# Kernel tuning notes

Hardware: AMD Instinct MI355X
Metric: run time of the kernel (lower is better)

The kernel has to match this reference:

```python
import jax, jax.numpy as jnp
import numpy as np

SPARQ = 32
NEG = -32000.0


def sparq_masked_bmm(a, b, xs, xs_mask, value):
    # a: [N,A,B], b: [N,C,B], xs/xs_mask: [N,A,Z]
    N, A, B = a.shape
    C = b.shape[1]
    xs = jnp.clip(xs, 0, C - 1)
    _, a_idx = jax.lax.top_k(jnp.abs(a), SPARQ)              # SparQ: keep top-32 |q| dims
    a_mask = jnp.zeros_like(a).at[
        jnp.arange(N)[:, None, None], jnp.arange(A)[None, :, None], a_idx].set(1.0)
    ts = jnp.einsum('nab,ncb->nac', a * a_mask, b)           # [N,A,C]
    ys = jnp.take_along_axis(ts, xs, axis=-1)                # [N,A,Z]
    return jnp.where(xs_mask > 0.5, ys, value)


def forward_mask(w0, k_budget, q, k):
    # q: [NH, A, HID], k: [NH, T_SRC, HID]; returns additive mask [NH, A, T_SRC]
    NH, A, HID = q.shape
    T_SRC = k.shape[1]
    start = T_SRC - A + 1
    tsrcs_f = jnp.arange(start, start + A).astype(jnp.float32)   # [A]
    ws = jnp.full((A,), float(w0), jnp.float32)
    Zc = 2 * k_budget + 8                                        # static cap on unique pixel count
    z = jnp.arange(Zc)
    pixels = jnp.broadcast_to(jnp.where(z < k_budget, z, 0)[None, None, :], (NH, A, Zc)).astype(jnp.int32)
    pmask = jnp.broadcast_to((z < w0).astype(jnp.float32)[None, None, :], (NH, A, Zc))
    need = (ws < tsrcs_f)[None, :, None]                         # computed ONCE, as in torch
    w = w0
    while True:  # static python loop: w doubles until T_SRC
        txs = jnp.round(pixels * (tsrcs_f / ws)[None, :, None]).astype(jnp.int32)
        scores = sparq_masked_bmm(q, k, txs, pmask, NEG)
        tks = jnp.clip(jnp.round(ws / tsrcs_f * k_budget), 1.0,
                       jnp.minimum(ws - 1.0, float(Zc - 1))).astype(jnp.int32)[None, :, None]
        _, idx = jax.lax.top_k(scores, Zc)
        new_pixels = jnp.take_along_axis(pixels, idx, axis=-1)
        new_mask = (z[None, None, :] < tks).astype(jnp.float32)
        pixels = jnp.where(need, new_pixels, pixels)
        pmask = jnp.where(need, new_mask, pmask)
        # tree doubling: each pixel splits into up to 2 children at the new scale
        ws_new = jnp.minimum(tsrcs_f, ws * 2.0)
        scale = (ws_new / ws)[None, :, None]
        ps_start = jnp.round(pixels * scale).astype(jnp.int32)
        ps_end = jnp.round((pixels + 1) * scale).astype(jnp.int32)
        counts = ps_end - ps_start
        reps = jnp.arange(2, dtype=jnp.float32)[None, None, None, :] * pmask[..., None]
        reps = jnp.minimum(reps, jnp.maximum(counts - 1, 0)[..., None].astype(jnp.float32)).astype(jnp.int32)
        ps = (ps_start[..., None] + reps).reshape(NH * A, Zc * 2)
        # emulate sort + unique_consecutive + compacting scatter (duplicates -> -1 tail)
        ps = jnp.sort(ps, axis=-1)
        is_new = jnp.concatenate([jnp.ones((NH * A, 1), bool), ps[:, 1:] != ps[:, :-1]], axis=1)
        rank = jnp.cumsum(is_new, axis=-1) - 1
        res = jnp.full_like(ps, -1).at[jnp.arange(NH * A)[:, None], rank].set(ps)
        res = res.reshape(NH, A, 2 * Zc)[:, :, :Zc]              # static truncation (valid count <= 2k+1)
        pmask = (res >= 0).astype(jnp.float32)
        pixels = jnp.where(res >= 0, res, 0)
        ws = ws_new
        if w == T_SRC:
            break
        w = min(T_SRC, w * 2)
    pixels = (pixels.astype(jnp.float32) * pmask).astype(jnp.int32)
    ret = jnp.full((NH, A, T_SRC), NEG, jnp.float32)
    ret = ret.at[jnp.arange(NH)[:, None, None], jnp.arange(A)[None, :, None], pixels].set(0.0)
    return ret


def tree_attention(q, k, v, mask, k_budget, w0):
    N, H, T_SRC, HID = k.shape
    T_DST = q.shape[2]
    t_dense = max(0, k_budget - T_SRC + T_DST)
    outs = []
    if t_dense > 0:
        s = jnp.einsum('nhqd,nhkd->nhqk', q[:, :, :t_dense], k) + mask[:, :, :t_dense]
        outs.append(jnp.einsum('nhqk,nhkd->nhqd', jax.nn.softmax(s, axis=-1), v))
    if T_DST - t_dense > 0:
        qs = q[:, :, t_dense:]
        ms = forward_mask(w0, k_budget,
                          qs.reshape(N * H, -1, HID),
                          k.reshape(N * H, T_SRC, HID)).reshape(N, H, -1, T_SRC)
        s = jnp.einsum('nhqd,nhkd->nhqk', qs, k) + mask[:, :, t_dense:] + ms
        outs.append(jnp.einsum('nhqk,nhkd->nhqd', jax.nn.softmax(s, axis=-1), v))
    return jnp.concatenate(outs, axis=2)


def setup_inputs():
    key = jax.random.key(0)
    kq, kk, kv = jax.random.split(key, 3)
    N, H, T, HID = 1, 8, 2048, 64
    q = jax.random.normal(kq, (N, H, T, HID), jnp.float32)
    k = jax.random.normal(kk, (N, H, T, HID), jnp.float32)
    v = jax.random.normal(kv, (N, H, T, HID), jnp.float32)
    causal = jnp.tril(jnp.ones((T, T), bool))
    mask = jnp.where(causal, 0.0, NEG)[None, None].astype(jnp.float32)
    return {"q": q, "k": k, "v": v, "mask": mask}


def reference(q, k, v, mask):
    return tree_attention(q, k, v, mask, 512, 64)
```

## Files before the change

kernel.cpp:

```cpp
#include <hip/hip_runtime.h>
#include <math.h>

constexpr int HID    = 64;
constexpr int TT     = 2048;
constexpr int NHEAD  = 8;
constexpr int TDENSE = 512;
constexpr int ZC     = 1032;
constexpr int BITW   = 1024;

__device__ __forceinline__ float waveSum(float v) {
#pragma unroll
    for (int o = 32; o > 0; o >>= 1) v += __shfl_xor(v, o, 64);
    return v;
}
__device__ __forceinline__ int waveSumI(int v) {
#pragma unroll
    for (int o = 32; o > 0; o >>= 1) v += __shfl_xor(v, o, 64);
    return v;
}
__device__ __forceinline__ float waveMax(float v) {
#pragma unroll
    for (int o = 32; o > 0; o >>= 1) v = fmaxf(v, __shfl_xor(v, o, 64));
    return v;
}
__device__ __forceinline__ unsigned orderKey(float f) {
    unsigned u = __float_as_uint(f);
    return (u & 0x80000000u) ? ~u : (u | 0x80000000u);
}
__device__ __forceinline__ float dot4(float4 a, float4 b) {
    return fmaf(a.x, b.x, fmaf(a.y, b.y, fmaf(a.z, b.z, a.w * b.w)));
}
__device__ __forceinline__ float dotRow64(const float4* __restrict__ kr,
                                          const float4* __restrict__ qs) {
    float s0 = 0.f, s1 = 0.f, s2 = 0.f, s3 = 0.f;
#pragma unroll 2
    for (int i = 0; i < 4; i++) {
        float4 ka = kr[4*i+0], kb = kr[4*i+1], kc = kr[4*i+2], kd = kr[4*i+3];
        float4 qa = qs[4*i+0], qb = qs[4*i+1], qc = qs[4*i+2], qd = qs[4*i+3];
        s0 += dot4(ka, qa); s1 += dot4(kb, qb);
        s2 += dot4(kc, qc); s3 += dot4(kd, qd);
    }
    return (s0 + s1) + (s2 + s3);
}

struct __align__(16) SMem {
    float qf[HID];
    float aq[HID];
    float qm[HID];
    float partial[256];
    unsigned short pixA[ZC];
    unsigned short pixB[ZC];
    unsigned skey[ZC];
    unsigned bitmap[BITW];
    unsigned hist[256];
    float red[8];
    int scal[8];
    unsigned wsum[4];
};

__global__ __launch_bounds__(256)
void tree_attn_kernel(const float* __restrict__ q, const float* __restrict__ k,
                      const float* __restrict__ v, float* __restrict__ out) {
    __shared__ SMem sm;
    const int t    = blockIdx.x;
    const int h    = blockIdx.y;
    const int tid  = threadIdx.x;
    const int lane = tid & 63;
    const int wave = tid >> 6;
    const int sub  = lane & 15;
    const int grp  = lane >> 4;

    const float* qrow = q + (size_t)(h * TT + t) * HID;
    const float* kh   = k + (size_t)h * TT * HID;
    const float* vh   = v + (size_t)h * TT * HID;
    float*       orow = out + (size_t)(h * TT + t) * HID;

    if (tid < HID) sm.qf[tid] = qrow[tid];
    __syncthreads();

    if (t < TDENSE) {
        const int nk = t + 1;
        float* f = (float*)sm.skey;
        for (int z = tid; z < nk; z += 256)
            f[z] = dotRow64((const float4*)(kh + (size_t)z * HID), (const float4*)sm.qf);
        __syncthreads();
        float m = -3.0e38f;
        for (int z = tid; z < nk; z += 256) m = fmaxf(m, f[z]);
        m = waveMax(m);
        if (lane == 0) sm.red[wave] = m;
        __syncthreads();
        m = fmaxf(fmaxf(sm.red[0], sm.red[1]), fmaxf(sm.red[2], sm.red[3]));
        __syncthreads();
        float ls = 0.f;
        for (int z = tid; z < nk; z += 256) { float e = expf(f[z] - m); f[z] = e; ls += e; }
        ls = waveSum(ls);
        if (lane == 0) sm.red[4 + wave] = ls;
        __syncthreads();
        ls = sm.red[4] + sm.red[5] + sm.red[6] + sm.red[7];
        float4 acc = {0.f, 0.f, 0.f, 0.f};
        for (int z = (wave << 2) + grp; z < nk; z += 16) {
            float w = f[z];
            const float4 vv = *reinterpret_cast<const float4*>(vh + (size_t)z * HID + (sub << 2));
            acc.x = fmaf(w, vv.x, acc.x); acc.y = fmaf(w, vv.y, acc.y);
            acc.z = fmaf(w, vv.z, acc.z); acc.w = fmaf(w, vv.w, acc.w);
        }
#pragma unroll
        for (int o = 16; o <= 32; o <<= 1) {
            acc.x += __shfl_xor(acc.x, o, 64); acc.y += __shfl_xor(acc.y, o, 64);
            acc.z += __shfl_xor(acc.z, o, 64); acc.w += __shfl_xor(acc.w, o, 64);
        }
        if (grp == 0) reinterpret_cast<float4*>(sm.partial)[wave * 16 + sub] = acc;
        __syncthreads();
        if (tid < HID) {
            float o = sm.partial[tid] + sm.partial[64 + tid] + sm.partial[128 + tid] + sm.partial[192 + tid];
            orow[tid] = o / ls;
        }
        return;
    }

    const int a     = t - TDENSE;
    const int tsrci = TDENSE + 1 + a;
    const float tsrc = (float)tsrci;

    if (tid < HID) sm.aq[tid] = fabsf(sm.qf[tid]);
    __syncthreads();
    if (tid < HID) {
        float me = sm.aq[tid]; int c = 0;
#pragma unroll
        for (int i = 0; i < HID; i++) {
            float o = sm.aq[i];
            c += (o > me) || (o == me && i < tid);
        }
        sm.qm[tid] = (c < 32) ? sm.qf[tid] : 0.0f;
    }
    for (int z = tid; z < ZC; z += 256) sm.pixA[z] = (z < 512) ? (unsigned short)z : (unsigned short)0;
    __syncthreads();

    unsigned short* cur = sm.pixA;
    unsigned short* nxt = sm.pixB;
    int U = 64;
    float ws = 64.0f;
    int pmaxb = 511;

    for (int it = 0; it < 6; it++) {
        if (ws == tsrc) break;
        const float wsn   = fminf(tsrc, ws * 2.0f);
        const float ratio = tsrc / ws;

        for (int z = tid; z < U; z += 256) {
            int p  = cur[z];
            int tx = (int)rintf((float)p * ratio);
            tx = min(max(tx, 0), TT - 1);
            float s = dotRow64((const float4*)(kh + (size_t)tx * HID), (const float4*)sm.qm);
            sm.skey[z] = orderKey(s);
        }
        float tkf = rintf((ws / tsrc) * 512.0f);
        tkf = fminf(fmaxf(tkf, 1.0f), fminf(ws - 1.0f, 1031.0f));
        const int tks = (int)tkf;
        __syncthreads();

        unsigned thr = 0u;
        if (tks < U) {
            if (tid == 0) { sm.scal[0] = tks; sm.scal[1] = 0; }
            __syncthreads();
            for (int bs = 24; bs >= 0; bs -= 8) {
                sm.hist[tid] = 0;
                __syncthreads();
                const unsigned pref = (unsigned)sm.scal[1];
                for (int z = tid; z < U; z += 256) {
                    unsigned key = sm.skey[z];
                    bool ok = (bs == 24) || ((key >> (bs + 8)) == (pref >> (bs + 8)));
                    if (ok) atomicAdd(&sm.hist[(key >> bs) & 255u], 1u);
                }
                __syncthreads();
                if (wave == 0) {
                    int c0 = (int)sm.hist[4*lane+0], c1 = (int)sm.hist[4*lane+1];
                    int c2 = (int)sm.hist[4*lane+2], c3 = (int)sm.hist[4*lane+3];
                    int tsum = c0 + c1 + c2 + c3;
                    int x = tsum;
#pragma unroll
                    for (int o = 1; o < 64; o <<= 1) {
                        int y = __shfl_up(x, o, 64);
                        if (lane >= o) x += y;
                    }
                    const int T   = __shfl(x, 63, 64);
                    const int wnt = sm.scal[0];
                    const int R   = T - wnt;
                    int p3 = x, p2 = p3 - c3, p1 = p2 - c2, p0 = p1 - c1, pm1 = p0 - c0;
                    int b = -1, nw = 0, cc = 0;
                    if      (p0 > R && pm1 <= R) { b = 4*lane+0; nw = p0 - R; cc = c0; }
                    else if (p1 > R && p0  <= R) { b = 4*lane+1; nw = p1 - R; cc = c1; }
                    else if (p2 > R && p1  <= R) { b = 4*lane+2; nw = p2 - R; cc = c2; }
                    else if (p3 > R && p2  <= R) { b = 4*lane+3; nw = p3 - R; cc = c3; }
                    if (b >= 0) {
                        sm.scal[0] = nw;
                        sm.scal[1] = (int)(pref | ((unsigned)b << bs));
                        sm.scal[2] = cc;
                    }
                }
                __syncthreads();
                if (sm.scal[2] == sm.scal[0]) break;
            }
            thr = (unsigned)sm.scal[1];
        }

        const float scale = wsn / ws;
        const int pmax_new = min(32767, (int)rintf((float)(pmaxb + 1) * scale));
        const int nwords = (pmax_new >> 5) + 1;
        for (int w0 = tid; w0 < nwords; w0 += 256) sm.bitmap[w0] = 0;
        __syncthreads();
        for (int z = tid; z < ZC; z += 256) {
            int p = cur[z];
            float pf = (float)p;
            int ps0 = (int)rintf(pf * scale);
            ps0 = min(ps0, 32767);
            atomicOr(&sm.bitmap[ps0 >> 5], 1u << (ps0 & 31));
            if (z < U && sm.skey[z] >= thr) {
                int ps1 = (int)rintf((pf + 1.0f) * scale);
                if (ps1 - ps0 >= 2) {
                    int ch = min(ps0 + 1, 32767);
                    atomicOr(&sm.bitmap[ch >> 5], 1u << (ch & 31));
                }
            }
        }
        __syncthreads();

        const int base = tid * 4;
        unsigned b0 = (base + 0 < nwords) ? sm.bitmap[base + 0] : 0u;
        unsigned b1 = (base + 1 < nwords) ? sm.bitmap[base + 1] : 0u;
        unsigned b2 = (base + 2 < nwords) ? sm.bitmap[base + 2] : 0u;
        unsigned b3 = (base + 3 < nwords) ? sm.bitmap[base + 3] : 0u;
        int myc = __popc(b0) + __popc(b1) + __popc(b2) + __popc(b3);
        int x = myc;
#pragma unroll
        for (int o = 1; o < 64; o <<= 1) {
            int y = __shfl_up(x, o, 64);
            if (lane >= o) x += y;
        }
        if (lane == 63) sm.wsum[wave] = (unsigned)x;
        __syncthreads();
        int wOff = 0;
        for (int wv = 0; wv < wave; wv++) wOff += (int)sm.wsum[wv];
        const int total = (int)(sm.wsum[0] + sm.wsum[1] + sm.wsum[2] + sm.wsum[3]);
        const int newU = min(total, ZC);
        int pos = wOff + x - myc;
#pragma unroll
        for (int w0 = 0; w0 < 4; w0++) {
            unsigned bits = (w0 == 0) ? b0 : (w0 == 1) ? b1 : (w0 == 2) ? b2 : b3;
            int vbase = (base + w0) << 5;
            while (bits) {
                int b = __ffs(bits) - 1;
                bits &= bits - 1;
                if (pos < ZC) nxt[pos] = (unsigned short)(vbase + b);
                pos++;
            }
        }
        for (int z = newU + tid; z < ZC; z += 256) nxt[z] = 0;
        __syncthreads();

        unsigned short* tmp = cur; cur = nxt; nxt = tmp;
        U = newU;
        ws = wsn;
        pmaxb = pmax_new;
    }

    int ca = 0;
    for (int z = tid; z < U; z += 256) ca += (cur[z] < tsrci) ? 1 : 0;
    ca = waveSumI(ca);
    if (lane == 0) sm.scal[wave] = ca;
    __syncthreads();
    const int Uatt = sm.scal[0] + sm.scal[1] + sm.scal[2] + sm.scal[3];
    __syncthreads();

    float* f = (float*)sm.skey;
    for (int z = tid; z < Uatt; z += 256)
        f[z] = dotRow64((const float4*)(kh + (size_t)cur[z] * HID), (const float4*)sm.qf);
    __syncthreads();
    float m = -3.0e38f;
    for (int z = tid; z < Uatt; z += 256) m = fmaxf(m, f[z]);
    m = waveMax(m);
    if (lane == 0) sm.red[wave] = m;
    __syncthreads();
    m = fmaxf(fmaxf(sm.red[0], sm.red[1]), fmaxf(sm.red[2], sm.red[3]));
    __syncthreads();
    float ls = 0.f;
    for (int z = tid; z < Uatt; z += 256) { float e = expf(f[z] - m); f[z] = e; ls += e; }
    ls = waveSum(ls);
    if (lane == 0) sm.red[4 + wave] = ls;
    __syncthreads();
    ls = sm.red[4] + sm.red[5] + sm.red[6] + sm.red[7];
    float4 acc = {0.f, 0.f, 0.f, 0.f};
    for (int z = (wave << 2) + grp; z < Uatt; z += 16) {
        float w = f[z];
        const float4 vv = *reinterpret_cast<const float4*>(vh + (size_t)cur[z] * HID + (sub << 2));
        acc.x = fmaf(w, vv.x, acc.x); acc.y = fmaf(w, vv.y, acc.y);
        acc.z = fmaf(w, vv.z, acc.z); acc.w = fmaf(w, vv.w, acc.w);
    }
#pragma unroll
    for (int o = 16; o <= 32; o <<= 1) {
        acc.x += __shfl_xor(acc.x, o, 64); acc.y += __shfl_xor(acc.y, o, 64);
        acc.z += __shfl_xor(acc.z, o, 64); acc.w += __shfl_xor(acc.w, o, 64);
    }
    if (grp == 0) reinterpret_cast<float4*>(sm.partial)[wave * 16 + sub] = acc;
    __syncthreads();
    if (tid < HID) {
        float o = sm.partial[tid] + sm.partial[64 + tid] + sm.partial[128 + tid] + sm.partial[192 + tid];
        orow[tid] = o / ls;
    }
}

extern "C" void kernel_launch(void* const* d_in, const int* in_sizes, int n_in,
                              void* d_out, int out_size, void* d_ws, size_t ws_size,
                              hipStream_t stream) {
    (void)in_sizes; (void)n_in; (void)d_ws; (void)ws_size; (void)out_size;
    const float* q = (const float*)d_in[0];
    const float* k = (const float*)d_in[1];
    const float* v = (const float*)d_in[2];
    float* out = (float*)d_out;
    dim3 grid(TT, NHEAD);
    tree_attn_kernel<<<grid, 256, 0, stream>>>(q, k, v, out);
}
```

Baseline: 1.171 ms.

## Fuse radix histogram into scoring, privatize per-wave hists, reverse block order, unroll dots

```diff
diff --git a/kernel.cpp b/kernel.cpp
--- a/kernel.cpp
+++ b/kernel.cpp
@@ -52,7 +52,7 @@
     unsigned short pixB[ZC];
     unsigned skey[ZC];
     unsigned bitmap[BITW];
-    unsigned hist[256];
+    unsigned hist[4][256];
     float red[8];
     int scal[8];
     unsigned wsum[4];
@@ -62,7 +62,7 @@
 void tree_attn_kernel(const float* __restrict__ q, const float* __restrict__ k,
                       const float* __restrict__ v, float* __restrict__ out) {
     __shared__ SMem sm;
-    const int t    = blockIdx.x;
+    const int t    = 2047 - (int)blockIdx.x;
     const int h    = blockIdx.y;
     const int tid  = threadIdx.x;
     const int lane = tid & 63;
@@ -81,8 +81,16 @@
     if (t < TDENSE) {
         const int nk = t + 1;
         float* f = (float*)sm.skey;
-        for (int z = tid; z < nk; z += 256)
-            f[z] = dotRow64((const float4*)(kh + (size_t)z * HID), (const float4*)sm.qf);
+        {
+            int z = tid;
+            for (; z + 256 < nk; z += 512) {
+                float s0 = dotRow64((const float4*)(kh + (size_t)z * HID), (const float4*)sm.qf);
+                float s1 = dotRow64((const float4*)(kh + (size_t)(z + 256) * HID), (const float4*)sm.qf);
+                f[z] = s0; f[z + 256] = s1;
+            }
+            if (z < nk)
+                f[z] = dotRow64((const float4*)(kh + (size_t)z * HID), (const float4*)sm.qf);
+        }
         __syncthreads();
         float m = -3.0e38f;
         for (int z = tid; z < nk; z += 256) m = fmaxf(m, f[z]);
@@ -134,6 +142,7 @@
         sm.qm[tid] = (c < 32) ? sm.qf[tid] : 0.0f;
     }
     for (int z = tid; z < ZC; z += 256) sm.pixA[z] = (z < 512) ? (unsigned short)z : (unsigned short)0;
+    for (int z = tid; z < 1024; z += 256) ((unsigned*)sm.hist)[z] = 0;
     __syncthreads();
 
     unsigned short* cur = sm.pixA;
@@ -147,12 +156,27 @@
         const float wsn   = fminf(tsrc, ws * 2.0f);
         const float ratio = tsrc / ws;
 
-        for (int z = tid; z < U; z += 256) {
-            int p  = cur[z];
-            int tx = (int)rintf((float)p * ratio);
-            tx = min(max(tx, 0), TT - 1);
-            float s = dotRow64((const float4*)(kh + (size_t)tx * HID), (const float4*)sm.qm);
-            sm.skey[z] = orderKey(s);
+        {
+            int z = tid;
+            for (; z + 256 < U; z += 512) {
+                int pA = cur[z], pB = cur[z + 256];
+                int txA = min(max((int)rintf((float)pA * ratio), 0), TT - 1);
+                int txB = min(max((int)rintf((float)pB * ratio), 0), TT - 1);
+                float sA = dotRow64((const float4*)(kh + (size_t)txA * HID), (const float4*)sm.qm);
+                float sB = dotRow64((const float4*)(kh + (size_t)txB * HID), (const float4*)sm.qm);
+                unsigned kA = orderKey(sA), kB = orderKey(sB);
+                sm.skey[z] = kA; sm.skey[z + 256] = kB;
+                atomicAdd(&sm.hist[wave][kA >> 24], 1u);
+                atomicAdd(&sm.hist[wave][kB >> 24], 1u);
+            }
+            if (z < U) {
+                int p  = cur[z];
+                int tx = min(max((int)rintf((float)p * ratio), 0), TT - 1);
+                float s = dotRow64((const float4*)(kh + (size_t)tx * HID), (const float4*)sm.qm);
+                unsigned kk2 = orderKey(s);
+                sm.skey[z] = kk2;
+                atomicAdd(&sm.hist[wave][kk2 >> 24], 1u);
+            }
         }
         float tkf = rintf((ws / tsrc) * 512.0f);
         tkf = fminf(fmaxf(tkf, 1.0f), fminf(ws - 1.0f, 1031.0f));
@@ -161,47 +185,57 @@
 
         unsigned thr = 0u;
         if (tks < U) {
-            if (tid == 0) { sm.scal[0] = tks; sm.scal[1] = 0; }
-            __syncthreads();
-            for (int bs = 24; bs >= 0; bs -= 8) {
-                sm.hist[tid] = 0;
-                __syncthreads();
-                const unsigned pref = (unsigned)sm.scal[1];
-                for (int z = tid; z < U; z += 256) {
-                    unsigned key = sm.skey[z];
-                    bool ok = (bs == 24) || ((key >> (bs + 8)) == (pref >> (bs + 8)));
-                    if (ok) atomicAdd(&sm.hist[(key >> bs) & 255u], 1u);
-                }
-                __syncthreads();
+            int bs = 24;
+            for (;;) {
                 if (wave == 0) {
-                    int c0 = (int)sm.hist[4*lane+0], c1 = (int)sm.hist[4*lane+1];
-                    int c2 = (int)sm.hist[4*lane+2], c3 = (int)sm.hist[4*lane+3];
-                    int tsum = c0 + c1 + c2 + c3;
-                    int x = tsum;
+                    const int i0 = 4 * lane;
+                    int c0 = 0, c1 = 0, c2 = 0, c3 = 0;
+#pragma unroll
+                    for (int w = 0; w < 4; w++) {
+                        c0 += (int)sm.hist[w][i0 + 0]; c1 += (int)sm.hist[w][i0 + 1];
+                        c2 += (int)sm.hist[w][i0 + 2]; c3 += (int)sm.hist[w][i0 + 3];
+                    }
+#pragma unroll
+                    for (int w = 0; w < 4; w++) {
+                        sm.hist[w][i0 + 0] = 0; sm.hist[w][i0 + 1] = 0;
+                        sm.hist[w][i0 + 2] = 0; sm.hist[w][i0 + 3] = 0;
+                    }
+                    const unsigned pref = (bs == 24) ? 0u : (unsigned)sm.scal[1];
+                    const int wnt = (bs == 24) ? tks : sm.scal[0];
+                    int x = c0 + c1 + c2 + c3;
 #pragma unroll
                     for (int o = 1; o < 64; o <<= 1) {
                         int y = __shfl_up(x, o, 64);
                         if (lane >= o) x += y;
                     }
-                    const int T   = __shfl(x, 63, 64);
-                    const int wnt = sm.scal[0];
-                    const int R   = T - wnt;
+                    const int T = __shfl(x, 63, 64);
+                    const int R = T - wnt;
                     int p3 = x, p2 = p3 - c3, p1 = p2 - c2, p0 = p1 - c1, pm1 = p0 - c0;
                     int b = -1, nw = 0, cc = 0;
-                    if      (p0 > R && pm1 <= R) { b = 4*lane+0; nw = p0 - R; cc = c0; }
-                    else if (p1 > R && p0  <= R) { b = 4*lane+1; nw = p1 - R; cc = c1; }
-                    else if (p2 > R && p1  <= R) { b = 4*lane+2; nw = p2 - R; cc = c2; }
-                    else if (p3 > R && p2  <= R) { b = 4*lane+3; nw = p3 - R; cc = c3; }
+                    if      (p0 > R && pm1 <= R) { b = i0 + 0; nw = p0 - R; cc = c0; }
+                    else if (p1 > R && p0  <= R) { b = i0 + 1; nw = p1 - R; cc = c1; }
+                    else if (p2 > R && p1  <= R) { b = i0 + 2; nw = p2 - R; cc = c2; }
+                    else if (p3 > R && p2  <= R) { b = i0 + 3; nw = p3 - R; cc = c3; }
                     if (b >= 0) {
                         sm.scal[0] = nw;
                         sm.scal[1] = (int)(pref | ((unsigned)b << bs));
                         sm.scal[2] = cc;
+                        sm.scal[3] = (cc == nw || bs == 0) ? 1 : 0;
                     }
                 }
                 __syncthreads();
-                if (sm.scal[2] == sm.scal[0]) break;
-            }
-            thr = (unsigned)sm.scal[1];
+                if (sm.scal[3]) { thr = (unsigned)sm.scal[1]; break; }
+                const unsigned pref = (unsigned)sm.scal[1];
+                bs -= 8;
+                for (int z = tid; z < U; z += 256) {
+                    unsigned key = sm.skey[z];
+                    if ((key >> (bs + 8)) == (pref >> (bs + 8)))
+                        atomicAdd(&sm.hist[wave][(key >> bs) & 255u], 1u);
+                }
+                __syncthreads();
+            }
+        } else {
+            for (int z = tid; z < 1024; z += 256) ((unsigned*)sm.hist)[z] = 0;
         }
 
         const float scale = wsn / ws;
@@ -267,14 +301,22 @@
     int ca = 0;
     for (int z = tid; z < U; z += 256) ca += (cur[z] < tsrci) ? 1 : 0;
     ca = waveSumI(ca);
-    if (lane == 0) sm.scal[wave] = ca;
-    __syncthreads();
-    const int Uatt = sm.scal[0] + sm.scal[1] + sm.scal[2] + sm.scal[3];
+    if (lane == 0) sm.scal[4 + wave] = ca;
+    __syncthreads();
+    const int Uatt = sm.scal[4] + sm.scal[5] + sm.scal[6] + sm.scal[7];
     __syncthreads();
 
     float* f = (float*)sm.skey;
-    for (int z = tid; z < Uatt; z += 256)
-        f[z] = dotRow64((const float4*)(kh + (size_t)cur[z] * HID), (const float4*)sm.qf);
+    {
+        int z = tid;
+        for (; z + 256 < Uatt; z += 512) {
+            float s0 = dotRow64((const float4*)(kh + (size_t)cur[z] * HID), (const float4*)sm.qf);
+            float s1 = dotRow64((const float4*)(kh + (size_t)cur[z + 256] * HID), (const float4*)sm.qf);
+            f[z] = s0; f[z + 256] = s1;
+        }
+        if (z < Uatt)
+            f[z] = dotRow64((const float4*)(kh + (size_t)cur[z] * HID), (const float4*)sm.qf);
+    }
     __syncthreads();
     float m = -3.0e38f;
     for (int z = tid; z < Uatt; z += 256) m = fmaxf(m, f[z]);
```

New measurement: 1.211 ms. 1.03x slower.
